# Performance work log

Measured on AMD Instinct MI355X. Metric: run time of the kernel, lower is better.

Reference implementation:

```python
import jax, jax.numpy as jnp
import numpy as np

NUM_TOKENS = 2048
HIDDEN = 2048
MOE_INTER = 1408
N_EXPERTS = 16
TOP_K = 4
N_SHARED = 2
SHARED_INTER = N_SHARED * MOE_INTER  # 2816
CAPACITY = 768
ROUTED_SCALE = 1.0


def setup_inputs() -> dict:
    key = jax.random.key(0)
    ks = jax.random.split(key, 9)
    s = 0.02  # init scale for stability
    return {
        "hidden_states": jax.random.normal(ks[0], (NUM_TOKENS, HIDDEN), jnp.float32),
        "w_gate": jax.random.normal(ks[1], (N_EXPERTS, HIDDEN), jnp.float32) * s,
        "w1": jax.random.normal(ks[2], (N_EXPERTS, HIDDEN, MOE_INTER), jnp.float32) * s,  # gate_proj
        "w3": jax.random.normal(ks[3], (N_EXPERTS, HIDDEN, MOE_INTER), jnp.float32) * s,  # up_proj
        "w2": jax.random.normal(ks[4], (N_EXPERTS, MOE_INTER, HIDDEN), jnp.float32) * s,  # down_proj
        "ws1": jax.random.normal(ks[5], (HIDDEN, SHARED_INTER), jnp.float32) * s,
        "ws3": jax.random.normal(ks[6], (HIDDEN, SHARED_INTER), jnp.float32) * s,
        "ws2": jax.random.normal(ks[7], (SHARED_INTER, HIDDEN), jnp.float32) * s,
    }


def _moe_forward(x, w_gate, w1, w3, w2, ws1, ws3, ws2):
    T, d = x.shape
    E = w1.shape[0]
    # ---- router: softmax scores, top-k selection (DeepSeek-V2, norm_topk_prob=False) ----
    scores = jax.nn.softmax(x @ w_gate.T, axis=-1)            # [T, E]
    topw, topi = jax.lax.top_k(scores, TOP_K)                 # [T, K]
    topw = topw * ROUTED_SCALE
    flat_e = topi.reshape(-1)                                 # [T*K] expert id per slot
    flat_w = topw.reshape(-1)                                 # [T*K]
    tok_ids = jnp.repeat(jnp.arange(T), TOP_K)                # [T*K]
    # ---- dispatch: position of each slot within its expert's buffer ----
    onehot = jax.nn.one_hot(flat_e, E, dtype=jnp.int32)       # [T*K, E]
    pos = jnp.take_along_axis(jnp.cumsum(onehot, axis=0), flat_e[:, None], axis=1)[:, 0] - 1
    valid = (pos < CAPACITY).astype(x.dtype)
    buf = jnp.zeros((E, CAPACITY, d), x.dtype).at[flat_e, pos].set(x[tok_ids], mode='drop')
    # ---- grouped SwiGLU expert FFN ----
    g = jnp.einsum('ecd,edi->eci', buf, w1)
    u = jnp.einsum('ecd,edi->eci', buf, w3)
    o = jnp.einsum('eci,eid->ecd', jax.nn.silu(g) * u, w2)    # [E, C, d]
    # ---- combine: gather back, weight, scatter-add per token ----
    gathered = o[flat_e, jnp.clip(pos, 0, CAPACITY - 1)] * (flat_w * valid)[:, None]
    routed = jax.ops.segment_sum(gathered, tok_ids, num_segments=T)  # [T, d]
    # ---- shared experts (always-on SwiGLU) ----
    shared = (jax.nn.silu(x @ ws1) * (x @ ws3)) @ ws2
    return routed + shared


def reference(hidden_states, w_gate, w1, w3, w2, ws1, ws3, ws2):
    return _moe_forward(hidden_states, w_gate, w1, w3, w2, ws1, ws3, ws2)
```

## Files before the change

### kernel.cpp

```cpp
#include <hip/hip_runtime.h>
#include <hip/hip_bf16.h>
#include <cstdint>

#define T_TOKENS 2048
#define HIDDEN 2048
#define INTER 1408
#define NEXP 16
#define TOPK 4
#define SINTER 2816
#define CAP 768
#define BK 32

typedef __attribute__((ext_vector_type(8))) short short8;
typedef __attribute__((ext_vector_type(8))) unsigned short ushort8;
typedef __attribute__((ext_vector_type(4))) float f32x4;

__device__ __forceinline__ float4 ld4f(const float* p) {
  return *reinterpret_cast<const float4*>(p);
}

__device__ __forceinline__ unsigned short f2bf(float v) {
  unsigned int u = __float_as_uint(v);
  unsigned int r = (u + 0x7FFFu + ((u >> 16) & 1u)) >> 16;
  return (unsigned short)r;
}

__device__ __forceinline__ void gld16(const void* g, void* l) {
  __builtin_amdgcn_global_load_lds(
      (const __attribute__((address_space(1))) void*)g,
      (__attribute__((address_space(3))) void*)l, 16, 0, 0);
}

__global__ __launch_bounds__(64) void router_kernel(
    const float* __restrict__ x, const float* __restrict__ wg,
    int* __restrict__ topi, float* __restrict__ topw,
    unsigned short* __restrict__ xb)
{
  const int t = blockIdx.x;
  const int lane = threadIdx.x;
  float acc[NEXP];
#pragma unroll
  for (int e = 0; e < NEXP; ++e) acc[e] = 0.f;
  const float* xr = x + (size_t)t * HIDDEN;
  unsigned short* xbr = xb + (size_t)t * HIDDEN;
  for (int i = lane; i < HIDDEN; i += 64) {
    float xv = xr[i];
    xbr[i] = f2bf(xv);
#pragma unroll
    for (int e = 0; e < NEXP; ++e) acc[e] += xv * wg[e * HIDDEN + i];
  }
#pragma unroll
  for (int e = 0; e < NEXP; ++e) {
#pragma unroll
    for (int off = 32; off > 0; off >>= 1)
      acc[e] += __shfl_xor(acc[e], off);
  }
  float m = acc[0];
#pragma unroll
  for (int e = 1; e < NEXP; ++e) m = fmaxf(m, acc[e]);
  float p[NEXP];
  float s = 0.f;
#pragma unroll
  for (int e = 0; e < NEXP; ++e) { p[e] = expf(acc[e] - m); s += p[e]; }
  const float inv = 1.f / s;
#pragma unroll
  for (int e = 0; e < NEXP; ++e) p[e] *= inv;
  if (lane == 0) {
#pragma unroll
    for (int k = 0; k < TOPK; ++k) {
      float best = -1.f; int bi = 0;
#pragma unroll
      for (int e = 0; e < NEXP; ++e)
        if (p[e] > best) { best = p[e]; bi = e; }
      topi[t * TOPK + k] = bi;
      topw[t * TOPK + k] = best;
      p[bi] = -1.f;
    }
  }
}

__global__ __launch_bounds__(1024) void partition_kernel(
    const int* __restrict__ topi, float* __restrict__ topw,
    int* __restrict__ rowtok, int* __restrict__ count)
{
  __shared__ int se[T_TOKENS * TOPK];
  for (int i = threadIdx.x; i < T_TOKENS * TOPK; i += 1024) se[i] = topi[i];
  __syncthreads();

  const int wave = threadIdx.x >> 6;
  const int lane = threadIdx.x & 63;
  const uint64_t below = (lane == 0) ? 0ull : ((~0ull) >> (64 - lane));
  int base = 0;
  for (int c = 0; c < T_TOKENS * TOPK; c += 64) {
    int ev = se[c + lane];
    uint64_t mask = __ballot(ev == wave);
    if (ev == wave) {
      int my = base + __popcll(mask & below);
      if (my < CAP) rowtok[wave * CAP + my] = c + lane;
      else          topw[c + lane] = 0.f;
    }
    base += __popcll(mask);
  }
  if (lane == 0) count[wave] = base < CAP ? base : CAP;
}

__global__ __launch_bounds__(256) void tcvt_w_kernel(
    const float* __restrict__ W0, const float* __restrict__ W1,
    unsigned short* __restrict__ T,
    int K, int N, long tz, int mul, int nz0, int which0, int which1)
{
  const int z = blockIdx.z;
  const float* W; int which; long zz;
  if (z < nz0) { W = W0; which = which0; zz = z; }
  else         { W = W1; which = which1; zz = z - nz0; }
  W += zz * (long)K * N;
  T += zz * tz;
  const int k0 = blockIdx.x * 64, n0 = blockIdx.y * 64;
  __shared__ float tile[64][65];
  const int tr = threadIdx.x >> 4;
  const int tc4 = (threadIdx.x & 15) * 4;
#pragma unroll
  for (int p = 0; p < 4; ++p) {
    int r = p * 16 + tr;
    float4 v = ld4f(W + (long)(k0 + r) * N + n0 + tc4);
    tile[r][tc4] = v.x; tile[r][tc4 + 1] = v.y;
    tile[r][tc4 + 2] = v.z; tile[r][tc4 + 3] = v.w;
  }
  __syncthreads();
  const int wn = threadIdx.x >> 3;
  const int wk = (threadIdx.x & 7) * 8;
#pragma unroll
  for (int p = 0; p < 2; ++p) {
    int n = p * 32 + wn;
    unsigned short o[8];
#pragma unroll
    for (int j = 0; j < 8; ++j) o[j] = f2bf(tile[wk + j][n]);
    const int gn = n0 + n;
    const long prow = ((long)(gn >> 4) * mul + which) * 16 + (gn & 15);
    *(ushort8*)(T + prow * K + k0 + wk) = *(ushort8*)&o[0];
  }
}

template<int NW, int EPI>
__global__ __launch_bounds__(NW * 64, (NW == 4) ? 3 : 2)
void gemm_bf(const unsigned short* __restrict__ Ag, int ldka,
             const unsigned short* __restrict__ Bg, long bstride,
             float* __restrict__ C, unsigned short* __restrict__ H, int ldc,
             const float* __restrict__ TW,
             const int* __restrict__ arows_g, int ashift, long aexp,
             const int* __restrict__ crows_g, long cexp,
             const int* __restrict__ cnt, int Mfix, int K,
             int MT, int NTn)
{
  constexpr int TN = NW * 32;
  constexpr int GA = 8 / NW;
  constexpr int WN = NW / 2;

  const int nwg = gridDim.x;
  const int lin = (blockIdx.x & 7) * (nwg >> 3) + (blockIdx.x >> 3);
  const int mt = lin % MT;
  const int rest = lin / MT;
  const int nt = rest % NTn;
  const int e = rest / NTn;

  const int M = cnt ? cnt[e] : Mfix;
  if (mt * 128 >= M) return;
  const int n0 = nt * TN;

  const int tid = threadIdx.x;
  const int l = tid & 63;
  const int w = tid >> 6;
  const int wm = w / WN;
  const int wn = w % WN;
  const int fr = l & 15;
  const int fc = l >> 4;

  const int* arows = arows_g ? arows_g + e * CAP : nullptr;
  const int* crows = crows_g ? crows_g + e * CAP : nullptr;
  const unsigned short* Bexp = Bg + (long)e * bstride;

  __shared__ __align__(16) unsigned short sA[3][128 * BK];
  __shared__ __align__(16) unsigned short sB[3][TN * BK];

  const int rb_s = ((l >> 3) & 1) | (((l >> 5) & 1) << 1);
  const int sch = ((l & 3) ^ rb_s) * 8;
  long aoff[GA], boff[2];
#pragma unroll
  for (int j = 0; j < GA; ++j) {
    const int rloc = (w * GA + j) * 16 + (l >> 2);
    int r = mt * 128 + rloc;
    if (r > M - 1) r = M - 1;
    const long arow = arows ? (long)(arows[r] >> ashift) : (aexp * e + r);
    aoff[j] = arow * (long)ldka + sch;
  }
#pragma unroll
  for (int j = 0; j < 2; ++j) {
    const int rloc = (w * 2 + j) * 16 + (l >> 2);
    boff[j] = (long)(n0 + rloc) * K + sch;
  }

  const int rb_r = ((fr >> 1) & 1) | (((fr >> 3) & 1) << 1);
  const int pcoff = (fc ^ rb_r) * 8;

  f32x4 acc[4][4];
#pragma unroll
  for (int i = 0; i < 4; ++i)
#pragma unroll
    for (int j = 0; j < 4; ++j) acc[i][j] = (f32x4)0.f;

  const int NT = K / BK;

  auto stage = [&](int buf, int kt) {
#pragma unroll
    for (int j = 0; j < GA; ++j)
      gld16(Ag + aoff[j] + kt, &sA[buf][(w * GA + j) * 16 * BK]);
#pragma unroll
    for (int j = 0; j < 2; ++j)
      gld16(Bexp + boff[j] + kt, &sB[buf][(w * 2 + j) * 16 * BK]);
  };

  stage(0, 0);
  stage(1, BK);

  int rb = 0, wb = 2;
  for (int t = 0; t < NT; ++t) {
    if (t + 1 < NT) {
      if constexpr (NW == 8) asm volatile("s_waitcnt vmcnt(3)" ::: "memory");
      else                   asm volatile("s_waitcnt vmcnt(4)" ::: "memory");
    } else {
      asm volatile("s_waitcnt vmcnt(0)" ::: "memory");
    }
    __builtin_amdgcn_s_barrier();
    __builtin_amdgcn_sched_barrier(0);

    if (t + 2 < NT) stage(wb, (t + 2) * BK);

    short8 fa[4], fb[4];
#pragma unroll
    for (int mi = 0; mi < 4; ++mi)
      fa[mi] = *(const short8*)&sA[rb][(wm * 64 + mi * 16 + fr) * BK + pcoff];
#pragma unroll
    for (int ni = 0; ni < 4; ++ni)
      fb[ni] = *(const short8*)&sB[rb][(wn * 64 + ni * 16 + fr) * BK + pcoff];
#pragma unroll
    for (int mi = 0; mi < 4; ++mi)
#pragma unroll
      for (int ni = 0; ni < 4; ++ni)
        acc[mi][ni] = __builtin_amdgcn_mfma_f32_16x16x32_bf16(fa[mi], fb[ni], acc[mi][ni], 0, 0, 0);

    rb = (rb == 2) ? 0 : rb + 1;
    wb = (wb == 2) ? 0 : wb + 1;
  }

#pragma unroll
  for (int mi = 0; mi < 4; ++mi)
#pragma unroll
    for (int rr = 0; rr < 4; ++rr) {
      const int r = mt * 128 + wm * 64 + mi * 16 + fc * 4 + rr;
      if (r >= M) continue;
      if constexpr (EPI == 2) {
        const long crow = crows ? (long)crows[r] : (cexp * e + r);
#pragma unroll
        for (int np = 0; np < 2; ++np) {
          const float g = acc[mi][2 * np][rr];
          const float u = acc[mi][2 * np + 1][rr];
          const float h = u * (g / (1.f + __expf(-g)));
          const int i = (n0 / 32 + wn * 2 + np) * 16 + fr;
          H[crow * (long)ldc + i] = f2bf(h);
        }
      } else if constexpr (EPI == 3) {
        const int slot = crows[r];
        const float wgt = TW[slot];
        if (wgt != 0.f) {
          const long tok = slot >> 2;
#pragma unroll
          for (int ni = 0; ni < 4; ++ni) {
            const int col = n0 + wn * 64 + ni * 16 + fr;
            atomicAdd(&C[tok * (long)ldc + col], wgt * acc[mi][ni][rr]);
          }
        }
      } else {
        const long crow = crows ? (long)crows[r] : (cexp * e + r);
#pragma unroll
        for (int ni = 0; ni < 4; ++ni) {
          const int col = n0 + wn * 64 + ni * 16 + fr;
          C[crow * (long)ldc + col] = acc[mi][ni][rr];
        }
      }
    }
}

extern "C" void kernel_launch(void* const* d_in, const int* in_sizes, int n_in,
                              void* d_out, int out_size, void* d_ws, size_t ws_size,
                              hipStream_t stream)
{
  const float* x   = (const float*)d_in[0];
  const float* wg  = (const float*)d_in[1];
  const float* w1  = (const float*)d_in[2];
  const float* w3  = (const float*)d_in[3];
  const float* w2  = (const float*)d_in[4];
  const float* ws1 = (const float*)d_in[5];
  const float* ws3 = (const float*)d_in[6];
  const float* ws2 = (const float*)d_in[7];
  float* out = (float*)d_out;

  char* w = (char*)d_ws;
  int*   topi   = (int*)w;   w += (size_t)T_TOKENS * TOPK * 4;
  float* topw   = (float*)w; w += (size_t)T_TOKENS * TOPK * 4;
  int*   rowtok = (int*)w;   w += (size_t)NEXP * CAP * 4;
  int*   count  = (int*)w;   w += 256;
  uintptr_t a = (uintptr_t)w; a = (a + 255) & ~(uintptr_t)255; w = (char*)a;

  const size_t XSZ  = (size_t)T_TOKENS * HIDDEN;
  const size_t WSI  = (size_t)2 * HIDDEN * SINTER;
  const size_t WRI  = (size_t)2 * NEXP * HIDDEN * INTER;
  const size_t HSSZ = (size_t)T_TOKENS * SINTER;
  const size_t HRSZ = (size_t)NEXP * CAP * INTER;

  unsigned short* xb  = (unsigned short*)w; w += XSZ * 2;
  unsigned short* wSi = (unsigned short*)w; w += WSI * 2;
  unsigned short* wRi = (unsigned short*)w; w += WRI * 2;
  unsigned short* hs  = (unsigned short*)w; w += HSSZ * 2;
  unsigned short* hr  = (unsigned short*)w; w += HRSZ * 2;
  unsigned short* wS2 = wSi;
  unsigned short* wR2 = wRi;

  router_kernel<<<T_TOKENS, 64, 0, stream>>>(x, wg, topi, topw, xb);
  partition_kernel<<<1, 1024, 0, stream>>>(topi, topw, rowtok, count);

  tcvt_w_kernel<<<dim3(HIDDEN / 64, SINTER / 64, 2), 256, 0, stream>>>(
      ws1, ws3, wSi, HIDDEN, SINTER, 0L, 2, 1, 0, 1);
  gemm_bf<4, 2><<<(T_TOKENS / 128) * (2 * SINTER / 128), 256, 0, stream>>>(
      xb, HIDDEN, wSi, 0L, nullptr, hs, SINTER, nullptr,
      nullptr, 0, 0L, nullptr, 0L,
      nullptr, T_TOKENS, HIDDEN, T_TOKENS / 128, 2 * SINTER / 128);

  tcvt_w_kernel<<<dim3(HIDDEN / 64, INTER / 64, 2 * NEXP), 256, 0, stream>>>(
      w1, w3, wRi, HIDDEN, INTER, (long)2 * HIDDEN * INTER, 2, NEXP, 0, 1);
  gemm_bf<4, 2><<<(CAP / 128) * (2 * INTER / 128) * NEXP, 256, 0, stream>>>(
      xb, HIDDEN, wRi, (long)2 * HIDDEN * INTER, nullptr, hr, INTER, nullptr,
      rowtok, 2, 0L, nullptr, (long)CAP,
      count, 0, HIDDEN, CAP / 128, 2 * INTER / 128);

  tcvt_w_kernel<<<dim3(SINTER / 64, HIDDEN / 64, 1), 256, 0, stream>>>(
      ws2, ws2, wS2, SINTER, HIDDEN, 0L, 1, 1, 0, 0);
  gemm_bf<4, 0><<<(T_TOKENS / 128) * (HIDDEN / 128), 256, 0, stream>>>(
      hs, SINTER, wS2, 0L, out, nullptr, HIDDEN, nullptr,
      nullptr, 0, 0L, nullptr, 0L,
      nullptr, T_TOKENS, SINTER, T_TOKENS / 128, HIDDEN / 128);

  tcvt_w_kernel<<<dim3(INTER / 64, HIDDEN / 64, NEXP), 256, 0, stream>>>(
      w2, w2, wR2, INTER, HIDDEN, (long)INTER * HIDDEN, 1, NEXP, 0, 0);
  gemm_bf<4, 3><<<(CAP / 128) * (HIDDEN / 128) * NEXP, 256, 0, stream>>>(
      hr, INTER, wR2, (long)INTER * HIDDEN, out, nullptr, HIDDEN, topw,
      nullptr, 0, (long)CAP, rowtok, 0L,
      count, 0, INTER, CAP / 128, HIDDEN / 128);
}
```

Before: 633.9 us.

## Add 256x256 eight-wave GEMM with 8-phase LDS pipeline for up/down projections

Adds a new 512-thread GEMM kernel that computes 256x256 output tiles with 64-wide K steps and double-buffered, XOR-swizzled LDS halves. Each iteration is split into eight phases that interleave global-to-LDS staging with MFMA work, with s_setprio raised around the MFMA blocks. The new kernel replaces the 128x128 kernel for the shared gate/up GEMM and for the routed up and down GEMMs, aiming for more data reuse per tile and better overlap of loads with compute. The shared down projection stays on a simplified 128-tile kernel. Larger tiles mean fewer workgroups, only one per CU, and more padded rows wasted on experts whose token counts are uneven.

```diff
diff --git a/kernel.cpp b/kernel.cpp
--- a/kernel.cpp
+++ b/kernel.cpp
@@ -141,21 +141,55 @@
   }
 }
 
-template<int NW, int EPI>
-__global__ __launch_bounds__(NW * 64, (NW == 4) ? 3 : 2)
-void gemm_bf(const unsigned short* __restrict__ Ag, int ldka,
-             const unsigned short* __restrict__ Bg, long bstride,
-             float* __restrict__ C, unsigned short* __restrict__ H, int ldc,
-             const float* __restrict__ TW,
-             const int* __restrict__ arows_g, int ashift, long aexp,
-             const int* __restrict__ crows_g, long cexp,
-             const int* __restrict__ cnt, int Mfix, int K,
-             int MT, int NTn)
-{
-  constexpr int TN = NW * 32;
-  constexpr int GA = 8 / NW;
-  constexpr int WN = NW / 2;
-
+#define PHASE8(D, MH, NH, STAGES, VMS)                                          \
+  {                                                                             \
+    short8 fa[4][2], fb[2][2];                                                  \
+    _Pragma("unroll")                                                           \
+    for (int mi = 0; mi < 4; ++mi)                                              \
+      _Pragma("unroll")                                                         \
+      for (int kk = 0; kk < 2; ++kk) {                                          \
+        const int idx = wm * 64 + mi * 16 + fr;                                 \
+        const int pc = (kk * 4 + fc) ^ (fr & 7);                                \
+        fa[mi][kk] = *(const short8*)&sA[D][MH][idx * 64 + pc * 8];             \
+      }                                                                         \
+    _Pragma("unroll")                                                           \
+    for (int ni = 0; ni < 2; ++ni)                                              \
+      _Pragma("unroll")                                                         \
+      for (int kk = 0; kk < 2; ++kk) {                                          \
+        const int idx = wn * 32 + ni * 16 + fr;                                 \
+        const int pc = (kk * 4 + fc) ^ (fr & 7);                                \
+        fb[ni][kk] = *(const short8*)&sB[D][NH][idx * 64 + pc * 8];             \
+      }                                                                         \
+    STAGES;                                                                     \
+    __builtin_amdgcn_s_barrier();                                               \
+    asm volatile("s_waitcnt lgkmcnt(0)" ::: "memory");                          \
+    __builtin_amdgcn_sched_barrier(0);                                          \
+    __builtin_amdgcn_s_setprio(1);                                              \
+    _Pragma("unroll")                                                           \
+    for (int mi = 0; mi < 4; ++mi)                                              \
+      _Pragma("unroll")                                                         \
+      for (int ni = 0; ni < 2; ++ni)                                            \
+        _Pragma("unroll")                                                       \
+        for (int kk = 0; kk < 2; ++kk)                                          \
+          acc[MH * 4 + mi][NH * 2 + ni] =                                       \
+              __builtin_amdgcn_mfma_f32_16x16x32_bf16(                          \
+                  fa[mi][kk], fb[ni][kk], acc[MH * 4 + mi][NH * 2 + ni], 0, 0, 0); \
+    __builtin_amdgcn_s_setprio(0);                                              \
+    VMS;                                                                        \
+    __builtin_amdgcn_s_barrier();                                               \
+  }
+
+template<int EPI>
+__global__ __launch_bounds__(512, 1)
+void gemm_bf8(const unsigned short* __restrict__ Ag, int ldka,
+              const unsigned short* __restrict__ Bg, long bstride,
+              float* __restrict__ C, unsigned short* __restrict__ H, int ldc,
+              const float* __restrict__ TW,
+              const int* __restrict__ arows_g, int ashift, long aexp,
+              const int* __restrict__ crows_g, long cexp,
+              const int* __restrict__ cnt, int Mfix, int K,
+              int MT, int NTn)
+{
   const int nwg = gridDim.x;
   const int lin = (blockIdx.x & 7) * (nwg >> 3) + (blockIdx.x >> 3);
   const int mt = lin % MT;
@@ -164,14 +198,14 @@
   const int e = rest / NTn;
 
   const int M = cnt ? cnt[e] : Mfix;
-  if (mt * 128 >= M) return;
-  const int n0 = nt * TN;
+  if (mt * 256 >= M) return;
+  const int n0 = nt * 256;
 
   const int tid = threadIdx.x;
   const int l = tid & 63;
   const int w = tid >> 6;
-  const int wm = w / WN;
-  const int wn = w % WN;
+  const int wm = w >> 2;
+  const int wn = w & 3;
   const int fr = l & 15;
   const int fc = l >> 4;
 
@@ -179,94 +213,86 @@
   const int* crows = crows_g ? crows_g + e * CAP : nullptr;
   const unsigned short* Bexp = Bg + (long)e * bstride;
 
-  __shared__ __align__(16) unsigned short sA[3][128 * BK];
-  __shared__ __align__(16) unsigned short sB[3][TN * BK];
-
-  const int rb_s = ((l >> 3) & 1) | (((l >> 5) & 1) << 1);
-  const int sch = ((l & 3) ^ rb_s) * 8;
-  long aoff[GA], boff[2];
-#pragma unroll
-  for (int j = 0; j < GA; ++j) {
-    const int rloc = (w * GA + j) * 16 + (l >> 2);
-    int r = mt * 128 + rloc;
-    if (r > M - 1) r = M - 1;
-    const long arow = arows ? (long)(arows[r] >> ashift) : (aexp * e + r);
-    aoff[j] = arow * (long)ldka + sch;
-  }
-#pragma unroll
-  for (int j = 0; j < 2; ++j) {
-    const int rloc = (w * 2 + j) * 16 + (l >> 2);
-    boff[j] = (long)(n0 + rloc) * K + sch;
-  }
-
-  const int rb_r = ((fr >> 1) & 1) | (((fr >> 3) & 1) << 1);
-  const int pcoff = (fc ^ rb_r) * 8;
-
-  f32x4 acc[4][4];
-#pragma unroll
-  for (int i = 0; i < 4; ++i)
+  __shared__ __align__(16) unsigned short sA[2][2][128 * 64];
+  __shared__ __align__(16) unsigned short sB[2][2][128 * 64];
+
+  const int sc = ((l & 7) ^ ((l >> 3) & 7)) * 8;
+  long aoffh[2][2], boffh[2][2];
+#pragma unroll
+  for (int h = 0; h < 2; ++h)
+#pragma unroll
+    for (int j = 0; j < 2; ++j) {
+      const int i = j * 64 + w * 8 + (l >> 3);
+      {
+        const int rt = ((i >> 6) << 7) + h * 64 + (i & 63);
+        int r = mt * 256 + rt;
+        if (r > M - 1) r = M - 1;
+        const long arow = arows ? (long)(arows[r] >> ashift) : (aexp * e + r);
+        aoffh[h][j] = arow * (long)ldka + sc;
+      }
+      {
+        const int ntc = ((i >> 5) << 6) + h * 32 + (i & 31);
+        boffh[h][j] = (long)(n0 + ntc) * K + sc;
+      }
+    }
+
+  f32x4 acc[8][4];
+#pragma unroll
+  for (int i = 0; i < 8; ++i)
 #pragma unroll
     for (int j = 0; j < 4; ++j) acc[i][j] = (f32x4)0.f;
 
-  const int NT = K / BK;
-
-  auto stage = [&](int buf, int kt) {
-#pragma unroll
-    for (int j = 0; j < GA; ++j)
-      gld16(Ag + aoff[j] + kt, &sA[buf][(w * GA + j) * 16 * BK]);
+  const int NT2 = K / 64;
+  const int NITER = NT2 / 2;
+
+  auto stgA = [&](int d, int h, int t) {
 #pragma unroll
     for (int j = 0; j < 2; ++j)
-      gld16(Bexp + boff[j] + kt, &sB[buf][(w * 2 + j) * 16 * BK]);
+      gld16(Ag + aoffh[h][j] + (long)t * 64, &sA[d][h][(j * 64 + w * 8) * 64]);
   };
-
-  stage(0, 0);
-  stage(1, BK);
-
-  int rb = 0, wb = 2;
-  for (int t = 0; t < NT; ++t) {
-    if (t + 1 < NT) {
-      if constexpr (NW == 8) asm volatile("s_waitcnt vmcnt(3)" ::: "memory");
-      else                   asm volatile("s_waitcnt vmcnt(4)" ::: "memory");
-    } else {
-      asm volatile("s_waitcnt vmcnt(0)" ::: "memory");
-    }
-    __builtin_amdgcn_s_barrier();
-    __builtin_amdgcn_sched_barrier(0);
-
-    if (t + 2 < NT) stage(wb, (t + 2) * BK);
-
-    short8 fa[4], fb[4];
-#pragma unroll
-    for (int mi = 0; mi < 4; ++mi)
-      fa[mi] = *(const short8*)&sA[rb][(wm * 64 + mi * 16 + fr) * BK + pcoff];
-#pragma unroll
-    for (int ni = 0; ni < 4; ++ni)
-      fb[ni] = *(const short8*)&sB[rb][(wn * 64 + ni * 16 + fr) * BK + pcoff];
-#pragma unroll
-    for (int mi = 0; mi < 4; ++mi)
-#pragma unroll
-      for (int ni = 0; ni < 4; ++ni)
-        acc[mi][ni] = __builtin_amdgcn_mfma_f32_16x16x32_bf16(fa[mi], fb[ni], acc[mi][ni], 0, 0, 0);
-
-    rb = (rb == 2) ? 0 : rb + 1;
-    wb = (wb == 2) ? 0 : wb + 1;
-  }
-
-#pragma unroll
-  for (int mi = 0; mi < 4; ++mi)
+  auto stgB = [&](int d, int h, int t) {
+#pragma unroll
+    for (int j = 0; j < 2; ++j)
+      gld16(Bexp + boffh[h][j] + (long)t * 64, &sB[d][h][(j * 64 + w * 8) * 64]);
+  };
+
+  stgA(0, 0, 0); stgB(0, 0, 0); stgA(0, 1, 0); stgB(0, 1, 0);
+  stgA(1, 0, 1); stgB(1, 0, 1);
+  asm volatile("s_waitcnt vmcnt(4)" ::: "memory");
+  __builtin_amdgcn_s_barrier();
+
+  for (int it = 0; it < NITER; ++it) {
+    const int t0 = 2 * it;
+    const bool nl = (it + 1 < NITER);
+    PHASE8(0, 0, 0, { stgB(1, 1, t0 + 1); stgA(1, 1, t0 + 1); }, (void)0);
+    PHASE8(0, 0, 1, (void)0, (void)0);
+    PHASE8(0, 1, 0, { if (t0 + 2 < NT2) stgA(0, 0, t0 + 2); }, (void)0);
+    PHASE8(0, 1, 1, { if (t0 + 2 < NT2) stgB(0, 0, t0 + 2); },
+           { if (nl) asm volatile("s_waitcnt vmcnt(4)" ::: "memory");
+             else    asm volatile("s_waitcnt vmcnt(0)" ::: "memory"); });
+    PHASE8(1, 0, 0, { if (t0 + 2 < NT2) { stgB(0, 1, t0 + 2); stgA(0, 1, t0 + 2); } }, (void)0);
+    PHASE8(1, 0, 1, (void)0, (void)0);
+    PHASE8(1, 1, 0, { if (t0 + 3 < NT2) stgA(1, 0, t0 + 3); }, (void)0);
+    PHASE8(1, 1, 1, { if (t0 + 3 < NT2) stgB(1, 0, t0 + 3); },
+           { if (nl) asm volatile("s_waitcnt vmcnt(4)" ::: "memory");
+             else    asm volatile("s_waitcnt vmcnt(0)" ::: "memory"); });
+  }
+
+#pragma unroll
+  for (int a = 0; a < 8; ++a)
 #pragma unroll
     for (int rr = 0; rr < 4; ++rr) {
-      const int r = mt * 128 + wm * 64 + mi * 16 + fc * 4 + rr;
+      const int r = mt * 256 + wm * 128 + (a >> 2) * 64 + (a & 3) * 16 + fc * 4 + rr;
       if (r >= M) continue;
       if constexpr (EPI == 2) {
         const long crow = crows ? (long)crows[r] : (cexp * e + r);
 #pragma unroll
-        for (int np = 0; np < 2; ++np) {
-          const float g = acc[mi][2 * np][rr];
-          const float u = acc[mi][2 * np + 1][rr];
-          const float h = u * (g / (1.f + __expf(-g)));
-          const int i = (n0 / 32 + wn * 2 + np) * 16 + fr;
-          H[crow * (long)ldc + i] = f2bf(h);
+        for (int nh = 0; nh < 2; ++nh) {
+          const float g = acc[a][nh * 2 + 0][rr];
+          const float u = acc[a][nh * 2 + 1][rr];
+          const float hv = u * (g / (1.f + __expf(-g)));
+          const int col = (n0 / 32 + wn * 2 + nh) * 16 + fr;
+          H[crow * (long)ldc + col] = f2bf(hv);
         }
       } else if constexpr (EPI == 3) {
         const int slot = crows[r];
@@ -274,18 +300,130 @@
         if (wgt != 0.f) {
           const long tok = slot >> 2;
 #pragma unroll
-          for (int ni = 0; ni < 4; ++ni) {
-            const int col = n0 + wn * 64 + ni * 16 + fr;
-            atomicAdd(&C[tok * (long)ldc + col], wgt * acc[mi][ni][rr]);
+          for (int nj = 0; nj < 4; ++nj) {
+            const int col = n0 + wn * 64 + nj * 16 + fr;
+            atomicAdd(&C[tok * (long)ldc + col], wgt * acc[a][nj][rr]);
           }
         }
       } else {
         const long crow = crows ? (long)crows[r] : (cexp * e + r);
 #pragma unroll
-        for (int ni = 0; ni < 4; ++ni) {
-          const int col = n0 + wn * 64 + ni * 16 + fr;
-          C[crow * (long)ldc + col] = acc[mi][ni][rr];
+        for (int nj = 0; nj < 4; ++nj) {
+          const int col = n0 + wn * 64 + nj * 16 + fr;
+          C[crow * (long)ldc + col] = acc[a][nj][rr];
         }
+      }
+    }
+}
+
+template<int EPI>
+__global__ __launch_bounds__(256, 2)
+void gemm_bf(const unsigned short* __restrict__ Ag, int ldka,
+             const unsigned short* __restrict__ Bg, long bstride,
+             float* __restrict__ C, unsigned short* __restrict__ H, int ldc,
+             const int* __restrict__ arows_g, int ashift, long aexp,
+             const int* __restrict__ crows_g, long cexp,
+             const int* __restrict__ cnt, int Mfix, int K,
+             int MT, int NTn)
+{
+  const int nwg = gridDim.x;
+  const int lin = (blockIdx.x & 7) * (nwg >> 3) + (blockIdx.x >> 3);
+  const int mt = lin % MT;
+  const int rest = lin / MT;
+  const int nt = rest % NTn;
+  const int e = rest / NTn;
+
+  const int M = cnt ? cnt[e] : Mfix;
+  if (mt * 128 >= M) return;
+  const int n0 = nt * 128;
+
+  const int tid = threadIdx.x;
+  const int l = tid & 63;
+  const int w = tid >> 6;
+  const int wm = w >> 1;
+  const int wn = w & 1;
+  const int fr = l & 15;
+  const int fc = l >> 4;
+
+  const int* arows = arows_g ? arows_g + e * CAP : nullptr;
+  const int* crows = crows_g ? crows_g + e * CAP : nullptr;
+  const unsigned short* Bexp = Bg + (long)e * bstride;
+
+  __shared__ __align__(16) unsigned short sA[3][128 * BK];
+  __shared__ __align__(16) unsigned short sB[3][128 * BK];
+
+  const int rb_s = ((l >> 3) & 1) | (((l >> 5) & 1) << 1);
+  const int sch = ((l & 3) ^ rb_s) * 8;
+  long aoff[2], boff[2];
+#pragma unroll
+  for (int j = 0; j < 2; ++j) {
+    const int rloc = j * 64 + w * 16 + (l >> 2);
+    int r = mt * 128 + rloc;
+    if (r > M - 1) r = M - 1;
+    const long arow = arows ? (long)(arows[r] >> ashift) : (aexp * e + r);
+    aoff[j] = arow * (long)ldka + sch;
+    boff[j] = (long)(n0 + rloc) * K + sch;
+  }
+
+  const int rb_r = ((fr >> 1) & 1) | (((fr >> 3) & 1) << 1);
+  const int pcoff = (fc ^ rb_r) * 8;
+
+  f32x4 acc[4][4];
+#pragma unroll
+  for (int i = 0; i < 4; ++i)
+#pragma unroll
+    for (int j = 0; j < 4; ++j) acc[i][j] = (f32x4)0.f;
+
+  const int NT = K / BK;
+
+  auto stage = [&](int buf, int kt) {
+#pragma unroll
+    for (int j = 0; j < 2; ++j) {
+      gld16(Ag + aoff[j] + kt, &sA[buf][(j * 64 + w * 16) * BK]);
+      gld16(Bexp + boff[j] + kt, &sB[buf][(j * 64 + w * 16) * BK]);
+    }
+  };
+
+  stage(0, 0);
+  stage(1, BK);
+
+  int rb = 0, wb = 2;
+  for (int t = 0; t < NT; ++t) {
+    if (t + 1 < NT) asm volatile("s_waitcnt vmcnt(4)" ::: "memory");
+    else            asm volatile("s_waitcnt vmcnt(0)" ::: "memory");
+    __builtin_amdgcn_s_barrier();
+    __builtin_amdgcn_sched_barrier(0);
+
+    if (t + 2 < NT) stage(wb, (t + 2) * BK);
+
+    short8 fa[4], fb[4];
+#pragma unroll
+    for (int mi = 0; mi < 4; ++mi)
+      fa[mi] = *(const short8*)&sA[rb][(wm * 64 + mi * 16 + fr) * BK + pcoff];
+#pragma unroll
+    for (int ni = 0; ni < 4; ++ni)
+      fb[ni] = *(const short8*)&sB[rb][(wn * 64 + ni * 16 + fr) * BK + pcoff];
+#pragma unroll
+    for (int mi = 0; mi < 4; ++mi)
+#pragma unroll
+      for (int ni = 0; ni < 4; ++ni)
+        acc[mi][ni] = __builtin_amdgcn_mfma_f32_16x16x32_bf16(fa[mi], fb[ni], acc[mi][ni], 0, 0, 0);
+
+    rb = (rb == 2) ? 0 : rb + 1;
+    wb = (wb == 2) ? 0 : wb + 1;
+  }
+
+#pragma unroll
+  for (int mi = 0; mi < 4; ++mi)
+#pragma unroll
+    for (int rr = 0; rr < 4; ++rr) {
+      const int r = mt * 128 + wm * 64 + mi * 16 + fc * 4 + rr;
+      if (r >= M) continue;
+      const long crow = crows ? (long)crows[r] : (cexp * e + r);
+#pragma unroll
+      for (int ni = 0; ni < 4; ++ni) {
+        const int col = n0 + wn * 64 + ni * 16 + fr;
+        C[crow * (long)ldc + col] = acc[mi][ni][rr];
       }
     }
 }
@@ -330,29 +468,29 @@
 
   tcvt_w_kernel<<<dim3(HIDDEN / 64, SINTER / 64, 2), 256, 0, stream>>>(
       ws1, ws3, wSi, HIDDEN, SINTER, 0L, 2, 1, 0, 1);
-  gemm_bf<4, 2><<<(T_TOKENS / 128) * (2 * SINTER / 128), 256, 0, stream>>>(
+  gemm_bf8<2><<<(T_TOKENS / 256) * (2 * SINTER / 256), 512, 0, stream>>>(
       xb, HIDDEN, wSi, 0L, nullptr, hs, SINTER, nullptr,
       nullptr, 0, 0L, nullptr, 0L,
-      nullptr, T_TOKENS, HIDDEN, T_TOKENS / 128, 2 * SINTER / 128);
+      nullptr, T_TOKENS, HIDDEN, T_TOKENS / 256, 2 * SINTER / 256);
 
   tcvt_w_kernel<<<dim3(HIDDEN / 64, INTER / 64, 2 * NEXP), 256, 0, stream>>>(
       w1, w3, wRi, HIDDEN, INTER, (long)2 * HIDDEN * INTER, 2, NEXP, 0, 1);
-  gemm_bf<4, 2><<<(CAP / 128) * (2 * INTER / 128) * NEXP, 256, 0, stream>>>(
+  gemm_bf8<2><<<(CAP / 256) * (2 * INTER / 256) * NEXP, 512, 0, stream>>>(
       xb, HIDDEN, wRi, (long)2 * HIDDEN * INTER, nullptr, hr, INTER, nullptr,
       rowtok, 2, 0L, nullptr, (long)CAP,
-      count, 0, HIDDEN, CAP / 128, 2 * INTER / 128);
+      count, 0, HIDDEN, CAP / 256, 2 * INTER / 256);
 
   tcvt_w_kernel<<<dim3(SINTER / 64, HIDDEN / 64, 1), 256, 0, stream>>>(
       ws2, ws2, wS2, SINTER, HIDDEN, 0L, 1, 1, 0, 0);
-  gemm_bf<4, 0><<<(T_TOKENS / 128) * (HIDDEN / 128), 256, 0, stream>>>(
-      hs, SINTER, wS2, 0L, out, nullptr, HIDDEN, nullptr,
+  gemm_bf<0><<<(T_TOKENS / 128) * (HIDDEN / 128), 256, 0, stream>>>(
+      hs, SINTER, wS2, 0L, out, nullptr, HIDDEN,
       nullptr, 0, 0L, nullptr, 0L,
       nullptr, T_TOKENS, SINTER, T_TOKENS / 128, HIDDEN / 128);
 
   tcvt_w_kernel<<<dim3(INTER / 64, HIDDEN / 64, NEXP), 256, 0, stream>>>(
       w2, w2, wR2, INTER, HIDDEN, (long)INTER * HIDDEN, 1, NEXP, 0, 0);
-  gemm_bf<4, 3><<<(CAP / 128) * (HIDDEN / 128) * NEXP, 256, 0, stream>>>(
+  gemm_bf8<3><<<(CAP / 256) * (HIDDEN / 256) * NEXP, 512, 0, stream>>>(
       hr, INTER, wR2, (long)INTER * HIDDEN, out, nullptr, HIDDEN, topw,
       nullptr, 0, (long)CAP, rowtok, 0L,
-      count, 0, INTER, CAP / 128, HIDDEN / 128);
-}
+      count, 0, INTER, CAP / 256, HIDDEN / 256);
+}
```

New measurement: 733.5 us. 15.7% more time.
